# Performance work log

Measured on AMD Instinct MI355X. Metric: run time of the kernel, lower is better.

## Reference

```python
import jax, jax.numpy as jnp
import numpy as np

BIN = 48
CPG = BIN * 3            # 144 hidden channels
SCALE = 2.0 / (BIN - 1)  # quantization step


def _causal_mask(k, include_center):
    # PixelCNN-style raster causal mask for a k x k kernel
    m = np.zeros((k, k), np.float32)
    c = k // 2
    m[:c, :] = 1.0
    m[c, :c] = 1.0
    if include_center:
        m[c, c] = 1.0
    return jnp.asarray(m)

MASK_NC = _causal_mask(5, False)  # first layer: strictly causal (exclude center)
MASK_C = _causal_mask(5, True)    # hidden/final layers: include center


def mconv(x, w, b, mask):
    # masked 5x5 conv, SAME padding, NCHW / OIHW
    y = jax.lax.conv_general_dilated(x, w * mask, (1, 1), 'SAME',
                                     dimension_numbers=('NCHW', 'OIHW', 'NCHW'))
    return y + b[None, :, None, None]


def setup_inputs() -> dict:
    key = jax.random.key(0)
    ks = jax.random.split(key, 8)
    H, W = 256, 512
    std = 0.02
    # quantized code in [-1, 1] on the bin grid, as produced by the decode loop
    lv = jax.random.randint(ks[0], (1, 1, H, W), 0, BIN)
    x = lv.astype(jnp.float32) * SCALE - 1.0
    return {
        'x': x,
        'w0': jax.random.normal(ks[1], (CPG, 1, 5, 5), jnp.float32) * std,
        'b0': jax.random.normal(ks[2], (CPG,), jnp.float32) * std,
        'wr': jax.random.normal(ks[3], (10, CPG, CPG, 5, 5), jnp.float32) * std,
        'br': jax.random.normal(ks[4], (10, CPG), jnp.float32) * std,
        'wf': jax.random.normal(ks[5], (BIN + 1, CPG, 5, 5), jnp.float32) * std,
        'bf': jax.random.normal(ks[6], (BIN + 1,), jnp.float32) * std,
    }


def reference(x, w0, b0, wr, br, wf, bf):
    # causal conv entropy network (CconvDc stack + 5 residual blocks)
    h = jax.nn.relu(mconv(x, w0, b0, MASK_NC))
    for i in range(5):  # EntropyResidualBlockD x5 (fixed small layer loop)
        y = jax.nn.relu(mconv(h, wr[2 * i], br[2 * i], MASK_C))
        y = jax.nn.relu(mconv(y, wr[2 * i + 1], br[2 * i + 1], MASK_C))
        h = h + y
    logits = mconv(h, wf, bf, MASK_C)            # (1, BIN+1, H, W)
    probs = jax.nn.softmax(logits, axis=1)       # per-pixel symbol distribution (EntropyTable input)

    # tail of forward: importance code -> channel mask -> depth-to-space x2
    tcode = jnp.floor((x + 1.0) / SCALE + 1e-5)  # (1,1,H,W) in [0, BIN-1]
    ch = jnp.arange(BIN * 4, dtype=x.dtype)[None, :, None, None]
    tmask = (ch < tcode * 4.0).astype(x.dtype)   # Imp2mask: (1, 4*BIN, H, W)
    N, C, H, W = tmask.shape
    t = tmask.reshape(N, C // 4, 2, 2, H, W)
    t = t.transpose(0, 1, 4, 2, 5, 3).reshape(N, C // 4, 2 * H, 2 * W)  # Dtow(2)
    return probs, t
```

## Files before the change

### kernel.cpp

```cpp
#include <hip/hip_runtime.h>
#include <hip/hip_bf16.h>
#include <stdint.h>

#define H 256
#define W 512
#define NCG 18
#define AW 520
#define AH 258
#define XB 16
#define ROWB (AW*XB)
#define CGB (AH*ROWB)
#define ACTB ((size_t)NCG*(size_t)CGB)
#define KG 236
#define NCHUNK 59
#define CHUNKB 9216
#define WPH_B ((size_t)KG*144*16)
#define WPF_B ((size_t)KG*64*16)

typedef float f32x4 __attribute__((ext_vector_type(4)));
typedef short bf16x8 __attribute__((ext_vector_type(8)));

__device__ __forceinline__ float bf2f(unsigned short u) {
  union { unsigned int i; float f; } v; v.i = ((unsigned int)u) << 16; return v.f;
}
__device__ __forceinline__ unsigned short f2bf(float f) {
  __hip_bfloat16 h = __float2bfloat16(f);
  return __builtin_bit_cast(unsigned short, h);
}
__device__ __forceinline__ void gload_lds16(const void* g, void* l) {
  __builtin_amdgcn_global_load_lds(
      (const __attribute__((address_space(1))) unsigned int*)g,
      (__attribute__((address_space(3))) unsigned int*)l, 16, 0, 0);
}

__global__ void k_pack_h(const float* __restrict__ wr, char* __restrict__ wph) {
  int idx = blockIdx.x * 256 + threadIdx.x;
  if (idx >= 10 * 144 * 144) return;
  int ci = idx % 144; int rem = idx / 144; int co = rem % 144; int layer = rem / 144;
  const float* src = wr + (size_t)((layer * 144 + co) * 144 + ci) * 25;
  unsigned short* dstL = (unsigned short*)(wph + (size_t)layer * WPH_B);
  int cig = ci >> 3, cis = ci & 7;
#pragma unroll
  for (int tap = 0; tap < 13; ++tap) {
    int ky = (tap >= 5) + (tap >= 10);
    int kx = tap - ky * 5;
    dstL[((size_t)(cig * 13 + tap) * 144 + co) * 8 + cis] = f2bf(src[ky * 5 + kx]);
  }
}
__global__ void k_pack_f(const float* __restrict__ wf, char* __restrict__ wpf) {
  int idx = blockIdx.x * 256 + threadIdx.x;
  if (idx >= 49 * 144) return;
  int ci = idx % 144; int co = idx / 144;
  const float* src = wf + (size_t)(co * 144 + ci) * 25;
  unsigned short* dst = (unsigned short*)wpf;
  int cig = ci >> 3, cis = ci & 7;
#pragma unroll
  for (int tap = 0; tap < 13; ++tap) {
    int ky = (tap >= 5) + (tap >= 10);
    int kx = tap - ky * 5;
    dst[((size_t)(cig * 13 + tap) * 64 + co) * 8 + cis] = f2bf(src[ky * 5 + kx]);
  }
}
__global__ void k_biaspad(const float* __restrict__ bf, float* __restrict__ bfp) {
  int i = threadIdx.x;
  bfp[i] = (i < 49) ? bf[i] : -1e30f;
}

__global__ void k_zeropad(char* __restrict__ actA, char* __restrict__ actB) {
  int i = blockIdx.x * 256 + threadIdx.x;
  if (i >= 2 * 18 * 2064) return;
  int s = i % 2064; int p = i / 2064; int cig = p % 18; int buf = p / 18;
  char* base = (buf ? actB : actA) + (size_t)cig * CGB;
  int row, colpx;
  if (s < 1040) { row = s / 520; colpx = s - row * 520; }
  else { int s2 = s - 1040; row = 2 + (s2 >> 2); int m = s2 & 3; colpx = (m < 2) ? m : (512 + m); }
  uint4 z; z.x = z.y = z.z = z.w = 0u;
  *(uint4*)(base + (size_t)row * ROWB + (size_t)colpx * 16) = z;
}

__global__ void k_layer0(const float* __restrict__ x, const float* __restrict__ w0,
                         const float* __restrict__ b0, char* __restrict__ act) {
  int i = blockIdx.x * 256 + threadIdx.x;
  int y = i >> 9, xx = i & 511;
  float xv[12];
#pragma unroll
  for (int tp = 0; tp < 12; ++tp) {
    int ky = (tp >= 5) + (tp >= 10);
    int kx = tp - ky * 5;
    int yy = y + ky - 2, xs = xx + kx - 2;
    bool ok = (yy >= 0) && (xs >= 0) && (xs < W);
    xv[tp] = ok ? x[yy * W + xs] : 0.f;
  }
  char* ob = act + (size_t)(y + 2) * ROWB + (size_t)(xx + 2) * XB;
  for (int cg = 0; cg < NCG; ++cg) {
    unsigned int us[4];
#pragma unroll
    for (int h2 = 0; h2 < 4; ++h2) {
      unsigned int lohi = 0;
#pragma unroll
      for (int p = 0; p < 2; ++p) {
        int co = cg * 8 + h2 * 2 + p;
        float a = b0[co];
#pragma unroll
        for (int tp = 0; tp < 12; ++tp) {
          int ky = (tp >= 5) + (tp >= 10);
          int kx = tp - ky * 5;
          a += w0[co * 25 + ky * 5 + kx] * xv[tp];
        }
        a = fmaxf(a, 0.f);
        lohi |= ((unsigned int)f2bf(a)) << (16 * p);
      }
      us[h2] = lohi;
    }
    uint4 v; v.x = us[0]; v.y = us[1]; v.z = us[2]; v.w = us[3];
    *(uint4*)(ob + (size_t)cg * CGB) = v;
  }
}

__global__ __launch_bounds__(256, 2)
void k_conv(const char* __restrict__ in, char* __restrict__ out,
            const char* __restrict__ wp, const float* __restrict__ bias, int res) {
  __shared__ __align__(16) char lA[2][CHUNKB];
  const int tid = threadIdx.x;
  const int wid = tid >> 6, lane = tid & 63;
  const int col = lane & 15, g = lane >> 4;

  int bid = blockIdx.x;
  int xcd = bid & 7, idx = bid >> 3;
  int by = xcd * 8 + (idx >> 3), bx = idx & 7;
  int y = by * 4 + wid, x0 = bx * 64;

  int pxo[4];
#pragma unroll
  for (int t = 0; t < 4; ++t) pxo[t] = (x0 + 16 * t + col) * XB;
  const char* bbase = in + (size_t)y * ROWB;

  f32x4 acc[9][4];
#pragma unroll
  for (int m = 0; m < 9; ++m)
#pragma unroll
    for (int t = 0; t < 4; ++t) acc[m][t] = (f32x4){0.f, 0.f, 0.f, 0.f};

  bf16x8 bA[4], bB[4];

  auto bload = [&](bf16x8 (&dst)[4], int c) __attribute__((always_inline)) {
    int kg = 4 * c + g;
    if (kg >= 234) kg = 0;
    int cig = kg / 13;
    int tap = kg - cig * 13;
    int ky = (tap >= 5) + (tap >= 10);
    int kx = tap - ky * 5;
    int off = cig * (int)CGB + ky * (int)ROWB + (kx << 4);
#pragma unroll
    for (int t = 0; t < 4; ++t) dst[t] = *(const bf16x8*)(bbase + (size_t)(off + pxo[t]));
  };

  auto stage = [&](char* ldsn, int c) __attribute__((always_inline)) {
    const char* wsrc = wp + (size_t)c * CHUNKB;
#pragma unroll
    for (int j0 = 0; j0 < 3; ++j0) {
      int j = wid + j0 * 4;
      if (j < 9) gload_lds16(wsrc + (size_t)j * 1024 + (lane << 4), ldsn + j * 1024);
    }
  };

  auto domfma = [&](const char* ldsc, bf16x8 (&bcur)[4]) __attribute__((always_inline)) {
    const char* abase = ldsc + ((g * 144 + col) << 4);
#pragma unroll
    for (int m = 0; m < 9; ++m) {
      bf16x8 a = *(const bf16x8*)(abase + m * 256);
#pragma unroll
      for (int t = 0; t < 4; ++t)
        acc[m][t] = __builtin_amdgcn_mfma_f32_16x16x32_bf16(a, bcur[t], acc[m][t], 0, 0, 0);
    }
  };

  auto phase = [&](const char* ldsc, char* ldsn, bf16x8 (&bcur)[4], bf16x8 (&bnext)[4],
                   int c) __attribute__((always_inline)) {
    stage(ldsn, c + 1);
    asm volatile("" ::: "memory");
    bload(bnext, c + 1);
    asm volatile("" ::: "memory");
    domfma(ldsc, bcur);
    asm volatile("s_waitcnt vmcnt(4)" ::: "memory");
    __builtin_amdgcn_s_barrier();
    asm volatile("" ::: "memory");
  };

  bload(bA, 0);
  stage(&lA[0][0], 0);
  asm volatile("s_waitcnt vmcnt(0)" ::: "memory");
  __builtin_amdgcn_s_barrier();
  asm volatile("" ::: "memory");

#pragma unroll 1
  for (int c = 0; c < NCHUNK - 1; c += 2) {
    phase(&lA[0][0], &lA[1][0], bA, bB, c);
    phase(&lA[1][0], &lA[0][0], bB, bA, c + 1);
  }
  domfma(&lA[0][0], bA);

  const int sub = (g & 1) * 8;
#pragma unroll
  for (int m = 0; m < 9; ++m) {
    int co0 = m * 16 + (g << 2);
    f32x4 bv = *(const f32x4*)(bias + co0);
    char* ob = out + (size_t)(co0 >> 3) * CGB + (size_t)(y + 2) * ROWB + sub + 32;
#pragma unroll
    for (int t = 0; t < 4; ++t) {
      char* oa = ob + pxo[t];
      float v0 = fmaxf(acc[m][t][0] + bv[0], 0.f);
      float v1 = fmaxf(acc[m][t][1] + bv[1], 0.f);
      float v2 = fmaxf(acc[m][t][2] + bv[2], 0.f);
      float v3 = fmaxf(acc[m][t][3] + bv[3], 0.f);
      if (res) {
        uint2 old = *(const uint2*)oa;
        v0 += bf2f((unsigned short)(old.x & 0xffff));
        v1 += bf2f((unsigned short)(old.x >> 16));
        v2 += bf2f((unsigned short)(old.y & 0xffff));
        v3 += bf2f((unsigned short)(old.y >> 16));
      }
      uint2 st;
      st.x = (unsigned int)f2bf(v0) | ((unsigned int)f2bf(v1) << 16);
      st.y = (unsigned int)f2bf(v2) | ((unsigned int)f2bf(v3) << 16);
      *(uint2*)oa = st;
    }
  }
}

__global__ __launch_bounds__(256, 2)
void k_convf(const char* __restrict__ in, float* __restrict__ probs,
             const char* __restrict__ wp, const float* __restrict__ bfp) {
  __shared__ __align__(16) char lA[2][4096];
  const int tid = threadIdx.x;
  const int wid = tid >> 6, lane = tid & 63;
  const int col = lane & 15, g = lane >> 4;

  int bid = blockIdx.x;
  int xcd = bid & 7, idx = bid >> 3;
  int by = xcd * 8 + (idx >> 3), bx = idx & 7;
  int y = by * 4 + wid, x0 = bx * 64;

  int pxo[4];
#pragma unroll
  for (int t = 0; t < 4; ++t) pxo[t] = (x0 + 16 * t + col) * XB;
  const char* bbase = in + (size_t)y * ROWB;

  f32x4 acc[4][4];
#pragma unroll
  for (int m = 0; m < 4; ++m)
#pragma unroll
    for (int t = 0; t < 4; ++t) acc[m][t] = (f32x4){0.f, 0.f, 0.f, 0.f};

  bf16x8 bA[4], bB[4];

  auto bload = [&](bf16x8 (&dst)[4], int c) __attribute__((always_inline)) {
    int kg = 4 * c + g;
    if (kg >= 234) kg = 0;
    int cig = kg / 13;
    int tap = kg - cig * 13;
    int ky = (tap >= 5) + (tap >= 10);
    int kx = tap - ky * 5;
    int off = cig * (int)CGB + ky * (int)ROWB + (kx << 4);
#pragma unroll
    for (int t = 0; t < 4; ++t) dst[t] = *(const bf16x8*)(bbase + (size_t)(off + pxo[t]));
  };

  auto stage = [&](char* ldsn, int c) __attribute__((always_inline)) {
    const char* wsrc = wp + (size_t)c * 4096;
    if (wid < 4) gload_lds16(wsrc + (size_t)wid * 1024 + (lane << 4), ldsn + wid * 1024);
  };

  auto domfma = [&](const char* ldsc, bf16x8 (&bcur)[4]) __attribute__((always_inline)) {
    const char* abase = ldsc + ((g * 64 + col) << 4);
#pragma unroll
    for (int m = 0; m < 4; ++m) {
      bf16x8 a = *(const bf16x8*)(abase + m * 256);
#pragma unroll
      for (int t = 0; t < 4; ++t)
        acc[m][t] = __builtin_amdgcn_mfma_f32_16x16x32_bf16(a, bcur[t], acc[m][t], 0, 0, 0);
    }
  };

  auto phase = [&](const char* ldsc, char* ldsn, bf16x8 (&bcur)[4], bf16x8 (&bnext)[4],
                   int c) __attribute__((always_inline)) {
    stage(ldsn, c + 1);
    asm volatile("" ::: "memory");
    bload(bnext, c + 1);
    asm volatile("" ::: "memory");
    domfma(ldsc, bcur);
    asm volatile("s_waitcnt vmcnt(4)" ::: "memory");
    __builtin_amdgcn_s_barrier();
    asm volatile("" ::: "memory");
  };

  bload(bA, 0);
  stage(&lA[0][0], 0);
  asm volatile("s_waitcnt vmcnt(0)" ::: "memory");
  __builtin_amdgcn_s_barrier();
  asm volatile("" ::: "memory");

#pragma unroll 1
  for (int c = 0; c < NCHUNK - 1; c += 2) {
    phase(&lA[0][0], &lA[1][0], bA, bB, c);
    phase(&lA[1][0], &lA[0][0], bB, bA, c + 1);
  }
  domfma(&lA[0][0], bA);

#pragma unroll
  for (int t = 0; t < 4; ++t) {
    float lg[4][4];
    float mx = -1e30f;
#pragma unroll
    for (int m = 0; m < 4; ++m) {
      f32x4 bv = *(const f32x4*)(bfp + m * 16 + (g << 2));
#pragma unroll
      for (int r = 0; r < 4; ++r) {
        lg[m][r] = acc[m][t][r] + bv[r];
        mx = fmaxf(mx, lg[m][r]);
      }
    }
    mx = fmaxf(mx, __shfl_xor(mx, 16));
    mx = fmaxf(mx, __shfl_xor(mx, 32));
    float s = 0.f;
#pragma unroll
    for (int m = 0; m < 4; ++m)
#pragma unroll
      for (int r = 0; r < 4; ++r) {
        lg[m][r] = __expf(lg[m][r] - mx);
        s += lg[m][r];
      }
    s += __shfl_xor(s, 16);
    s += __shfl_xor(s, 32);
    float inv = 1.f / s;
    int xp = x0 + 16 * t + col;
    float* op = probs + (size_t)y * W + xp;
#pragma unroll
    for (int m = 0; m < 4; ++m)
#pragma unroll
      for (int r = 0; r < 4; ++r) {
        int co = m * 16 + (g << 2) + r;
        if (co < 49) op[(size_t)co * (H * W)] = lg[m][r] * inv;
      }
  }
}

__global__ void k_tmask(const float* __restrict__ x, float* __restrict__ out1) {
  int i = blockIdx.x * 256 + threadIdx.x;
  int yy = i >> 10, xx = i & 1023;
  float xv = x[(yy >> 1) * W + (xx >> 1)];
  float tc = floorf((xv + 1.0f) / (float)(2.0 / 47.0) + 1e-5f);
#pragma unroll 4
  for (int g = 0; g < 48; ++g)
    out1[(size_t)g * (512 * 1024) + i] = ((float)g < tc) ? 1.0f : 0.0f;
}

extern "C" void kernel_launch(void* const* d_in, const int* in_sizes, int n_in,
                              void* d_out, int out_size, void* d_ws, size_t ws_size,
                              hipStream_t stream) {
  const float* x  = (const float*)d_in[0];
  const float* w0 = (const float*)d_in[1];
  const float* b0 = (const float*)d_in[2];
  const float* wr = (const float*)d_in[3];
  const float* br = (const float*)d_in[4];
  const float* wf = (const float*)d_in[5];
  const float* bf = (const float*)d_in[6];

  char* ws   = (char*)d_ws;
  char* actA = ws;
  char* actB = ws + ACTB;
  char* wph  = ws + 2 * ACTB;
  char* wpf  = wph + 10 * WPH_B;
  float* bfp = (float*)(wpf + WPF_B);

  hipMemsetAsync(wph, 0, 10 * WPH_B + WPF_B + 256, stream);
  k_zeropad<<<(2 * 18 * 2064 + 255) / 256, 256, 0, stream>>>(actA, actB);

  k_pack_h<<<(10 * 144 * 144 + 255) / 256, 256, 0, stream>>>(wr, wph);
  k_pack_f<<<(49 * 144 + 255) / 256, 256, 0, stream>>>(wf, wpf);
  k_biaspad<<<1, 64, 0, stream>>>(bf, bfp);

  k_layer0<<<512, 256, 0, stream>>>(x, w0, b0, actA);

  for (int i = 0; i < 5; ++i) {
    k_conv<<<512, 256, 0, stream>>>(actA, actB, wph + (size_t)(2 * i) * WPH_B,
                                    br + (2 * i) * 144, 0);
    k_conv<<<512, 256, 0, stream>>>(actB, actA, wph + (size_t)(2 * i + 1) * WPH_B,
                                    br + (2 * i + 1) * 144, 1);
  }

  float* probs = (float*)d_out;
  k_convf<<<512, 256, 0, stream>>>(actA, probs, wpf, bfp);
  k_tmask<<<2048, 256, 0, stream>>>(x, probs + (size_t)49 * H * W);
}
```

Baseline: 744.8 us.

## Switch conv kernels to single-wave blocks without barriers, incremental tap indexing, setprio

Each conv block now holds a single 64-thread wave that stages its own copy of each weight chunk into LDS, so the workgroup barriers between chunks go away. The per-chunk division that computed the tap and channel-group offset is replaced by an incrementally updated tap counter. s_setprio is raised around the MFMA loop. In exchange, every wave now loads all the weights itself, with no sharing across four waves, which quadruples weight traffic into LDS and may lower occupancy because of LDS use per wave.

```diff
diff --git a/kernel.cpp b/kernel.cpp
--- a/kernel.cpp
+++ b/kernel.cpp
@@ -14,6 +14,7 @@
 #define KG 236
 #define NCHUNK 59
 #define CHUNKB 9216
+#define CHUNKFB 4096
 #define WPH_B ((size_t)KG*144*16)
 #define WPF_B ((size_t)KG*64*16)
 
@@ -117,18 +118,17 @@
   }
 }
 
-__global__ __launch_bounds__(256, 2)
+__global__ __launch_bounds__(64, 2)
 void k_conv(const char* __restrict__ in, char* __restrict__ out,
             const char* __restrict__ wp, const float* __restrict__ bias, int res) {
   __shared__ __align__(16) char lA[2][CHUNKB];
-  const int tid = threadIdx.x;
-  const int wid = tid >> 6, lane = tid & 63;
+  const int lane = threadIdx.x & 63;
   const int col = lane & 15, g = lane >> 4;
 
   int bid = blockIdx.x;
   int xcd = bid & 7, idx = bid >> 3;
-  int by = xcd * 8 + (idx >> 3), bx = idx & 7;
-  int y = by * 4 + wid, x0 = bx * 64;
+  int y = xcd * 32 + (idx >> 3);
+  int x0 = (idx & 7) * 64;
 
   int pxo[4];
 #pragma unroll
@@ -143,29 +143,26 @@
 
   bf16x8 bA[4], bB[4];
 
-  auto bload = [&](bf16x8 (&dst)[4], int c) __attribute__((always_inline)) {
-    int kg = 4 * c + g;
-    if (kg >= 234) kg = 0;
-    int cig = kg / 13;
-    int tap = kg - cig * 13;
+  int tap = g, offc = 0;
+  auto bload = [&](bf16x8 (&dst)[4]) __attribute__((always_inline)) {
     int ky = (tap >= 5) + (tap >= 10);
     int kx = tap - ky * 5;
-    int off = cig * (int)CGB + ky * (int)ROWB + (kx << 4);
+    int off = offc + ky * (int)ROWB + (kx << 4);
 #pragma unroll
     for (int t = 0; t < 4; ++t) dst[t] = *(const bf16x8*)(bbase + (size_t)(off + pxo[t]));
+    tap += 4; if (tap >= 13) { tap -= 13; offc += (int)CGB; }
   };
 
   auto stage = [&](char* ldsn, int c) __attribute__((always_inline)) {
     const char* wsrc = wp + (size_t)c * CHUNKB;
 #pragma unroll
-    for (int j0 = 0; j0 < 3; ++j0) {
-      int j = wid + j0 * 4;
-      if (j < 9) gload_lds16(wsrc + (size_t)j * 1024 + (lane << 4), ldsn + j * 1024);
-    }
+    for (int j = 0; j < 9; ++j)
+      gload_lds16(wsrc + (size_t)j * 1024 + (lane << 4), ldsn + j * 1024);
   };
 
   auto domfma = [&](const char* ldsc, bf16x8 (&bcur)[4]) __attribute__((always_inline)) {
     const char* abase = ldsc + ((g * 144 + col) << 4);
+    __builtin_amdgcn_s_setprio(1);
 #pragma unroll
     for (int m = 0; m < 9; ++m) {
       bf16x8 a = *(const bf16x8*)(abase + m * 256);
@@ -173,25 +170,23 @@
       for (int t = 0; t < 4; ++t)
         acc[m][t] = __builtin_amdgcn_mfma_f32_16x16x32_bf16(a, bcur[t], acc[m][t], 0, 0, 0);
     }
+    __builtin_amdgcn_s_setprio(0);
   };
 
   auto phase = [&](const char* ldsc, char* ldsn, bf16x8 (&bcur)[4], bf16x8 (&bnext)[4],
                    int c) __attribute__((always_inline)) {
     stage(ldsn, c + 1);
     asm volatile("" ::: "memory");
-    bload(bnext, c + 1);
+    bload(bnext);
     asm volatile("" ::: "memory");
     domfma(ldsc, bcur);
     asm volatile("s_waitcnt vmcnt(4)" ::: "memory");
-    __builtin_amdgcn_s_barrier();
-    asm volatile("" ::: "memory");
-  };
-
-  bload(bA, 0);
+  };
+
   stage(&lA[0][0], 0);
-  asm volatile("s_waitcnt vmcnt(0)" ::: "memory");
-  __builtin_amdgcn_s_barrier();
   asm volatile("" ::: "memory");
+  bload(bA);
+  asm volatile("s_waitcnt vmcnt(4)" ::: "memory");
 
 #pragma unroll 1
   for (int c = 0; c < NCHUNK - 1; c += 2) {
@@ -228,18 +223,17 @@
   }
 }
 
-__global__ __launch_bounds__(256, 2)
+__global__ __launch_bounds__(64, 2)
 void k_convf(const char* __restrict__ in, float* __restrict__ probs,
              const char* __restrict__ wp, const float* __restrict__ bfp) {
-  __shared__ __align__(16) char lA[2][4096];
-  const int tid = threadIdx.x;
-  const int wid = tid >> 6, lane = tid & 63;
+  __shared__ __align__(16) char lA[2][CHUNKFB];
+  const int lane = threadIdx.x & 63;
   const int col = lane & 15, g = lane >> 4;
 
   int bid = blockIdx.x;
   int xcd = bid & 7, idx = bid >> 3;
-  int by = xcd * 8 + (idx >> 3), bx = idx & 7;
-  int y = by * 4 + wid, x0 = bx * 64;
+  int y = xcd * 32 + (idx >> 3);
+  int x0 = (idx & 7) * 64;
 
   int pxo[4];
 #pragma unroll
@@ -254,25 +248,26 @@
 
   bf16x8 bA[4], bB[4];
 
-  auto bload = [&](bf16x8 (&dst)[4], int c) __attribute__((always_inline)) {
-    int kg = 4 * c + g;
-    if (kg >= 234) kg = 0;
-    int cig = kg / 13;
-    int tap = kg - cig * 13;
+  int tap = g, offc = 0;
+  auto bload = [&](bf16x8 (&dst)[4]) __attribute__((always_inline)) {
     int ky = (tap >= 5) + (tap >= 10);
     int kx = tap - ky * 5;
-    int off = cig * (int)CGB + ky * (int)ROWB + (kx << 4);
+    int off = offc + ky * (int)ROWB + (kx << 4);
 #pragma unroll
     for (int t = 0; t < 4; ++t) dst[t] = *(const bf16x8*)(bbase + (size_t)(off + pxo[t]));
+    tap += 4; if (tap >= 13) { tap -= 13; offc += (int)CGB; }
   };
 
   auto stage = [&](char* ldsn, int c) __attribute__((always_inline)) {
-    const char* wsrc = wp + (size_t)c * 4096;
-    if (wid < 4) gload_lds16(wsrc + (size_t)wid * 1024 + (lane << 4), ldsn + wid * 1024);
+    const char* wsrc = wp + (size_t)c * CHUNKFB;
+#pragma unroll
+    for (int j = 0; j < 4; ++j)
+      gload_lds16(wsrc + (size_t)j * 1024 + (lane << 4), ldsn + j * 1024);
   };
 
   auto domfma = [&](const char* ldsc, bf16x8 (&bcur)[4]) __attribute__((always_inline)) {
     const char* abase = ldsc + ((g * 64 + col) << 4);
+    __builtin_amdgcn_s_setprio(1);
 #pragma unroll
     for (int m = 0; m < 4; ++m) {
       bf16x8 a = *(const bf16x8*)(abase + m * 256);
@@ -280,25 +275,23 @@
       for (int t = 0; t < 4; ++t)
         acc[m][t] = __builtin_amdgcn_mfma_f32_16x16x32_bf16(a, bcur[t], acc[m][t], 0, 0, 0);
     }
+    __builtin_amdgcn_s_setprio(0);
   };
 
   auto phase = [&](const char* ldsc, char* ldsn, bf16x8 (&bcur)[4], bf16x8 (&bnext)[4],
                    int c) __attribute__((always_inline)) {
     stage(ldsn, c + 1);
     asm volatile("" ::: "memory");
-    bload(bnext, c + 1);
+    bload(bnext);
     asm volatile("" ::: "memory");
     domfma(ldsc, bcur);
     asm volatile("s_waitcnt vmcnt(4)" ::: "memory");
-    __builtin_amdgcn_s_barrier();
-    asm volatile("" ::: "memory");
-  };
-
-  bload(bA, 0);
+  };
+
   stage(&lA[0][0], 0);
-  asm volatile("s_waitcnt vmcnt(0)" ::: "memory");
-  __builtin_amdgcn_s_barrier();
   asm volatile("" ::: "memory");
+  bload(bA);
+  asm volatile("s_waitcnt vmcnt(4)" ::: "memory");
 
 #pragma unroll 1
   for (int c = 0; c < NCHUNK - 1; c += 2) {
@@ -383,13 +376,13 @@
   k_layer0<<<512, 256, 0, stream>>>(x, w0, b0, actA);
 
   for (int i = 0; i < 5; ++i) {
-    k_conv<<<512, 256, 0, stream>>>(actA, actB, wph + (size_t)(2 * i) * WPH_B,
+    k_conv<<<2048, 64, 0, stream>>>(actA, actB, wph + (size_t)(2 * i) * WPH_B,
                                     br + (2 * i) * 144, 0);
-    k_conv<<<512, 256, 0, stream>>>(actB, actA, wph + (size_t)(2 * i + 1) * WPH_B,
+    k_conv<<<2048, 64, 0, stream>>>(actB, actA, wph + (size_t)(2 * i + 1) * WPH_B,
                                     br + (2 * i + 1) * 144, 1);
   }
 
   float* probs = (float*)d_out;
-  k_convf<<<512, 256, 0, stream>>>(actA, probs, wpf, bfp);
+  k_convf<<<2048, 64, 0, stream>>>(actA, probs, wpf, bfp);
   k_tmask<<<2048, 256, 0, stream>>>(x, probs + (size_t)49 * H * W);
 }
```

After: 802.9 us. 1.08x slower.
